# Optimization experiments

Measured on AMD Instinct MI355X. Metric: run time of the kernel, lower is better.

## Reference

```python
import jax, jax.numpy as jnp
import numpy as np

T, D, H, HD = 2048, 2048, 16, 128
ROPE_BASE = 10000.0
NEG = jnp.float32(-1e30)


def rms_norm(x):
    # F.rms_norm(x, (x.size(-1),)) with default eps = dtype eps
    eps = jnp.finfo(x.dtype).eps
    return x * jax.lax.rsqrt(jnp.mean(x * x, axis=-1, keepdims=True) + eps)


def rotary(x):
    # x: [1, T, H, hd]; half-split rotation as in Rotary.forward
    hd = x.shape[-1]
    inv_freq = (1.0 / ROPE_BASE) ** (jnp.arange(0, hd, 2, dtype=jnp.float32) / hd)
    t = jnp.arange(x.shape[1], dtype=jnp.float32)
    freqs = jnp.outer(t, inv_freq)                      # [T, hd/2]
    cos = jnp.cos(freqs)[None, :, None, :]
    sin = jnp.sin(freqs)[None, :, None, :]
    x1, x2 = jnp.split(x, 2, axis=-1)
    return jnp.concatenate([x1 * cos + x2 * sin, -x1 * sin + x2 * cos], axis=-1)


def setup_inputs() -> dict:
    key = jax.random.key(0)
    ks = jax.random.split(key, 10)
    w = lambda k, shape: jax.random.normal(k, shape, jnp.float32) * 0.02
    return {
        "x":  jax.random.normal(ks[0], (1, T, D), jnp.float32),
        "vi": jax.random.normal(ks[1], (1, T, H, HD), jnp.float32),
        "x0": jax.random.normal(ks[2], (1, T, D), jnp.float32),
        "wq": w(ks[3], (D, D)),
        "wk": w(ks[4], (D, D)),
        "wv": w(ks[5], (D, D)),
        "wo": w(ks[6], (D, D)),
        "lamb": jnp.float32(0.5),
        "lambdas": jnp.array([1.0, 0.0], jnp.float32),
        "w_fc": w(ks[7], (4 * D, D)),
        "w_proj": w(ks[8], (D, 4 * D)),
    }


def reference(x, vi, x0, wq, wk, wv, wo, lamb, lambdas, w_fc, w_proj):
    # Block: residual blend with initial embedding x0
    xb = lambdas[0] * x + lambdas[1] * x0
    xn = rms_norm(xb)

    # --- CausalSelfAttention ---
    q = (xn @ wq.T).reshape(1, T, H, HD)
    k = (xn @ wk.T).reshape(1, T, H, HD)
    v = (xn @ wv.T).reshape(1, T, H, HD)
    v = (1.0 - lamb) * v + lamb * vi                     # value-embedding blend
    q = rotary(rms_norm(q))
    k = rotary(rms_norm(k))

    scale = 1.0 / jnp.sqrt(jnp.float32(HD))              # flex_attention default scale
    scores = jnp.einsum('bqhd,bkhd->bhqk', q, k) * scale # [1,H,T,T]
    causal = jnp.tril(jnp.ones((T, T), bool))
    scores = jnp.where(causal[None, None], scores, NEG)
    attn = jax.nn.softmax(scores, axis=-1)
    y = jnp.einsum('bhqk,bkhd->bqhd', attn, v).reshape(1, T, D)
    a = y @ wo.T                                         # attention output REPLACES x (no residual)

    # --- MLP with squared ReLU ---
    h = rms_norm(a) @ w_fc.T
    h = jnp.square(jax.nn.relu(h))
    out = a + h @ w_proj.T
    return out
```

## Files before the change

### kernel.cpp

```cpp
#include <hip/hip_runtime.h>
#include <hip/hip_bf16.h>

typedef __bf16 bf16;
typedef __bf16 bf16x8 __attribute__((ext_vector_type(8)));
typedef float f32x4 __attribute__((ext_vector_type(4)));

#define DD 2048
#define DD2 4194304ull
#define G9_LDS 131072

__device__ __forceinline__ void glds16(const void* g, void* l) {
  __builtin_amdgcn_global_load_lds((const __attribute__((address_space(1))) void*)g,
                                   (__attribute__((address_space(3))) void*)l, 16, 0, 0);
}

__device__ __forceinline__ f32x4 mfma16(bf16x8 a, bf16x8 b, f32x4 c) {
  return __builtin_amdgcn_mfma_f32_16x16x32_bf16(a, b, c, 0, 0, 0);
}

__global__ __launch_bounds__(256) void cvt_all(const float* __restrict__ s0, const float* __restrict__ s1,
                                               const float* __restrict__ s2, const float* __restrict__ s3,
                                               const float* __restrict__ s4, const float* __restrict__ s5,
                                               bf16* __restrict__ dbase) {
  const int b = blockIdx.x;
  const float* src; bf16* dst; int lb;
  if (b < 8192)       { int r = b >> 11; src = (r == 0) ? s0 : (r == 1) ? s1 : (r == 2) ? s2 : s3;
                        dst = dbase + (size_t)r * DD2; lb = b & 2047; }
  else if (b < 16384) { src = s4; dst = dbase + 4 * DD2; lb = b - 8192; }
  else                { src = s5; dst = dbase + 8 * DD2; lb = b - 16384; }
  size_t i = ((size_t)lb * 256 + threadIdx.x) * 8;
  float4 a = *(const float4*)(src + i);
  float4 c = *(const float4*)(src + i + 4);
  bf16x8 o;
  o[0] = (bf16)a.x; o[1] = (bf16)a.y; o[2] = (bf16)a.z; o[3] = (bf16)a.w;
  o[4] = (bf16)c.x; o[5] = (bf16)c.y; o[6] = (bf16)c.z; o[7] = (bf16)c.w;
  *(bf16x8*)(dst + i) = o;
}

template<bool BLEND>
__global__ __launch_bounds__(256) void prenorm_k(const float* __restrict__ x, const float* __restrict__ x0,
                                                 const float* __restrict__ lambdas, bf16* __restrict__ out) {
  const int t = blockIdx.x, tid = threadIdx.x;
  const float4* xr = (const float4*)(x + (size_t)t * DD);
  float4 a0 = xr[2 * tid], a1 = xr[2 * tid + 1];
  float v[8] = {a0.x, a0.y, a0.z, a0.w, a1.x, a1.y, a1.z, a1.w};
  if (BLEND) {
    const float l0 = lambdas[0], l1 = lambdas[1];
    const float4* yr = (const float4*)(x0 + (size_t)t * DD);
    float4 b0 = yr[2 * tid], b1 = yr[2 * tid + 1];
    float w[8] = {b0.x, b0.y, b0.z, b0.w, b1.x, b1.y, b1.z, b1.w};
#pragma unroll
    for (int i = 0; i < 8; ++i) v[i] = l0 * v[i] + l1 * w[i];
  }
  float ss = 0.f;
#pragma unroll
  for (int i = 0; i < 8; ++i) ss += v[i] * v[i];
#pragma unroll
  for (int off = 1; off < 64; off <<= 1) ss += __shfl_xor(ss, off, 64);
  __shared__ float red[4];
  const int wid = tid >> 6;
  if ((tid & 63) == 0) red[wid] = ss;
  __syncthreads();
  ss = red[0] + red[1] + red[2] + red[3];
  const float sc = rsqrtf(ss * (1.0f / DD) + 1.1920928955078125e-07f);
  bf16x8 o;
#pragma unroll
  for (int i = 0; i < 8; ++i) o[i] = (bf16)(v[i] * sc);
  *(bf16x8*)(out + (size_t)t * DD + tid * 8) = o;
}

__global__ __launch_bounds__(256) void rope_k(bf16* __restrict__ qg, bf16* __restrict__ kg) {
  const int tid = threadIdx.x, lane = tid & 63, wid = tid >> 6;
  const int p = blockIdx.x * 4 + wid;
  bf16* base = ((p >> 15) ? kg : qg);
  const int t = (p >> 4) & 2047, hh = p & 15;
  base += (size_t)t * DD + hh * 128;
  float x1 = (float)base[lane], x2 = (float)base[lane + 64];
  float ss = x1 * x1 + x2 * x2;
#pragma unroll
  for (int off = 1; off < 64; off <<= 1) ss += __shfl_xor(ss, off, 64);
  const float sc = rsqrtf(ss * (1.0f / 128.0f) + 1.1920928955078125e-07f);
  x1 *= sc; x2 *= sc;
  const float fr = (float)t * exp2f((float)lane * (-13.287712379549449f / 64.0f));
  const float s = sinf(fr), c = cosf(fr);
  base[lane]      = (bf16)(x1 * c + x2 * s);
  base[lane + 64] = (bf16)(-x1 * s + x2 * c);
}

__global__ __launch_bounds__(256) void vt_k(const bf16* __restrict__ v, bf16* __restrict__ vt) {
  __shared__ alignas(16) bf16 tile[16 * 128];
  const int tb = blockIdx.x, hb = blockIdx.y, tid = threadIdx.x;
  glds16(v + (size_t)(tb * 16 + (tid >> 4)) * DD + hb * 128 + (tid & 15) * 8, tile + tid * 8);
  __syncthreads();
  const int d_l = tid & 127, tc = tid >> 7;
  bf16x8 o;
#pragma unroll
  for (int i = 0; i < 8; ++i) o[i] = tile[(tc * 8 + i) * 128 + d_l];
  *(bf16x8*)(vt + (size_t)(hb * 128 + d_l) * DD + tb * 16 + tc * 8) = o;
}

__device__ __forceinline__ void g9_stageA(const bf16* A, int Kstride, int row0, int k0,
                                          bf16* buf, int hm, int tid) {
#pragma unroll
  for (int i = 0; i < 2; ++i) {
    int e = tid + i * 512;
    int prl = e >> 3, slot = e & 7;
    int wm = prl >> 6, r63 = prl & 63;
    glds16(A + (size_t)(row0 + wm * 128 + hm * 64 + r63) * Kstride + k0 + ((slot ^ (prl & 7)) * 8),
           buf + hm * 8192 + e * 8);
  }
}
__device__ __forceinline__ void g9_stageB(const bf16* B, int Kstride, int col0, int k0,
                                          bf16* buf, int hn, int tid) {
#pragma unroll
  for (int i = 0; i < 2; ++i) {
    int e = tid + i * 512;
    int pbl = e >> 3, slot = e & 7;
    int wn = pbl >> 5, q = pbl & 31;
    glds16(B + (size_t)(col0 + wn * 64 + hn * 32 + q) * Kstride + k0 + ((slot ^ (pbl & 7)) * 8),
           buf + 16384 + hn * 8192 + e * 8);
  }
}

__device__ __forceinline__ void gemm9_core(const bf16* __restrict__ A, const bf16* __restrict__ B,
                                           int Kstride, int Klen, int row0, int col0,
                                           bf16* smem, f32x4 (&acc)[8][4]) {
  const int tid = threadIdx.x, lane = tid & 63, wid = tid >> 6;
  const int wm = wid >> 2, wn = wid & 3;
  const int l15 = lane & 15, g = lane >> 4;
  const int sw = l15 & 7;
  const int NT = Klen >> 6;
  g9_stageA(A, Kstride, row0, 0, smem, 0, tid);
  g9_stageB(B, Kstride, col0, 0, smem, 0, tid);
  g9_stageB(B, Kstride, col0, 0, smem, 1, tid);
  g9_stageA(A, Kstride, row0, 0, smem, 1, tid);

  bf16x8 a[4][2], b0[2][2], b1[2][2];
  for (int t = 0; t < NT; ++t) {
    bf16* cb = smem + (t & 1) * 32768;
    bf16* sb = smem + ((t + 1) & 1) * 32768;
    const int ks0 = (t + 1) << 6;
    const bool st = (t + 1) < NT;
    asm volatile("s_waitcnt vmcnt(4)" ::: "memory");
    __builtin_amdgcn_s_barrier();
#pragma unroll
    for (int mm = 0; mm < 4; ++mm)
#pragma unroll
      for (int ks = 0; ks < 2; ++ks) {
        int pr = wm * 64 + mm * 16 + l15;
        a[mm][ks] = *(const bf16x8*)(cb + pr * 64 + (((ks * 4 + g) ^ sw) * 8));
      }
#pragma unroll
    for (int nn = 0; nn < 2; ++nn)
#pragma unroll
      for (int ks = 0; ks < 2; ++ks) {
        int pb = wn * 32 + nn * 16 + l15;
        b0[nn][ks] = *(const bf16x8*)(cb + 16384 + pb * 64 + (((ks * 4 + g) ^ sw) * 8));
      }
    if (st) g9_stageA(A, Kstride, row0, ks0, sb, 0, tid);
    __builtin_amdgcn_s_setprio(1);
#pragma unroll
    for (int mm = 0; mm < 4; ++mm)
#pragma unroll
      for (int nn = 0; nn < 2; ++nn)
#pragma unroll
        for (int ks = 0; ks < 2; ++ks)
          acc[mm][nn] = mfma16(a[mm][ks], b0[nn][ks], acc[mm][nn]);
    __builtin_amdgcn_s_setprio(0);
    __builtin_amdgcn_s_barrier();
    if (st) { asm volatile("s_waitcnt vmcnt(4)" ::: "memory"); }
    else    { asm volatile("s_waitcnt vmcnt(2)" ::: "memory"); }
    __builtin_amdgcn_s_barrier();
#pragma unroll
    for (int nn = 0; nn < 2; ++nn)
#pragma unroll
      for (int ks = 0; ks < 2; ++ks) {
        int pb = 128 + wn * 32 + nn * 16 + l15;
        b1[nn][ks] = *(const bf16x8*)(cb + 16384 + pb * 64 + (((ks * 4 + g) ^ sw) * 8));
      }
    if (st) g9_stageB(B, Kstride, col0, ks0, sb, 0, tid);
    __builtin_amdgcn_s_setprio(1);
#pragma unroll
    for (int mm = 0; mm < 4; ++mm)
#pragma unroll
      for (int nn = 0; nn < 2; ++nn)
#pragma unroll
        for (int ks = 0; ks < 2; ++ks)
          acc[mm][2 + nn] = mfma16(a[mm][ks], b1[nn][ks], acc[mm][2 + nn]);
    __builtin_amdgcn_s_setprio(0);
    __builtin_amdgcn_s_barrier();
    if (st) { asm volatile("s_waitcnt vmcnt(4)" ::: "memory"); }
    else    { asm volatile("s_waitcnt vmcnt(0)" ::: "memory"); }
    __builtin_amdgcn_s_barrier();
#pragma unroll
    for (int mm = 0; mm < 4; ++mm)
#pragma unroll
      for (int ks = 0; ks < 2; ++ks) {
        int pr = 128 + wm * 64 + mm * 16 + l15;
        a[mm][ks] = *(const bf16x8*)(cb + pr * 64 + (((ks * 4 + g) ^ sw) * 8));
      }
    if (st) g9_stageB(B, Kstride, col0, ks0, sb, 1, tid);
    __builtin_amdgcn_s_setprio(1);
#pragma unroll
    for (int mm = 0; mm < 4; ++mm)
#pragma unroll
      for (int nn = 0; nn < 2; ++nn)
#pragma unroll
        for (int ks = 0; ks < 2; ++ks)
          acc[4 + mm][nn] = mfma16(a[mm][ks], b0[nn][ks], acc[4 + mm][nn]);
    __builtin_amdgcn_s_setprio(0);
    __builtin_amdgcn_s_barrier();
    if (st) g9_stageA(A, Kstride, row0, ks0, sb, 1, tid);
    __builtin_amdgcn_s_setprio(1);
#pragma unroll
    for (int mm = 0; mm < 4; ++mm)
#pragma unroll
      for (int nn = 0; nn < 2; ++nn)
#pragma unroll
        for (int ks = 0; ks < 2; ++ks)
          acc[4 + mm][2 + nn] = mfma16(a[mm][ks], b1[nn][ks], acc[4 + mm][2 + nn]);
    __builtin_amdgcn_s_setprio(0);
    __builtin_amdgcn_s_barrier();
  }
}

#define GEMM9_EPI(STMT)                                                        \
  { const int lane_ = threadIdx.x & 63, wid_ = threadIdx.x >> 6;               \
    const int l15_ = lane_ & 15, g_ = lane_ >> 4;                              \
    const int wm_ = wid_ >> 2, wn_ = wid_ & 3;                                 \
    _Pragma("unroll") for (int m = 0; m < 8; ++m)                              \
    _Pragma("unroll") for (int n = 0; n < 4; ++n)                              \
    _Pragma("unroll") for (int j = 0; j < 4; ++j) {                            \
      int grow = row0 + wm_ * 128 + (m >> 2) * 64 + (m & 3) * 16 + g_ * 4 + j; \
      int gcol = col0 + wn_ * 64 + (n >> 1) * 32 + (n & 1) * 16 + l15_;        \
      float vacc = acc[m][n][j];                                               \
      STMT; } }

__global__ __launch_bounds__(512, 1) void gemm9_qkv(const bf16* __restrict__ A,
    const bf16* __restrict__ Wq, const bf16* __restrict__ Wk, const bf16* __restrict__ Wv,
    bf16* __restrict__ oq, bf16* __restrict__ ok, bf16* __restrict__ ov,
    const float* __restrict__ vi, const float* __restrict__ lambp) {
  extern __shared__ bf16 smem9[];
  const int z = blockIdx.z;
  const bf16* B = (z == 0) ? Wq : (z == 1) ? Wk : Wv;
  bf16* out = (z == 0) ? oq : (z == 1) ? ok : ov;
  const int row0 = blockIdx.y * 256, col0 = blockIdx.x * 256;
  f32x4 acc[8][4] = {};
  gemm9_core(A, B, DD, DD, row0, col0, smem9, acc);
  if (z < 2) {
    GEMM9_EPI( out[(size_t)grow * DD + gcol] = (bf16)vacc; )
  } else {
    const float lam = *lambp;
    GEMM9_EPI( out[(size_t)grow * DD + gcol] =
                 (bf16)((1.0f - lam) * vacc + lam * vi[(size_t)grow * DD + gcol]); )
  }
}

template<int EPI>
__global__ __launch_bounds__(512, 1) void gemm9_ep(const bf16* __restrict__ A, const bf16* __restrict__ B,
                                                   void* __restrict__ outv, int N, int Kstride,
                                                   int KlenMain, int Ktot) {
  extern __shared__ bf16 smem9[];
  const int row0 = blockIdx.y * 256, col0 = blockIdx.x * 256;
  const int kofs = blockIdx.z * KlenMain;
  const int Klen = min(KlenMain, Ktot - kofs);
  f32x4 acc[8][4] = {};
  gemm9_core(A + kofs, B + kofs, Kstride, Klen, row0, col0, smem9, acc);
  if (EPI == 2) { float* out = (float*)outv + (size_t)blockIdx.z * DD2;
    GEMM9_EPI( out[(size_t)grow * N + gcol] = vacc; ) }
  if (EPI == 3) { bf16* out = (bf16*)outv;
    GEMM9_EPI( float r = fmaxf(vacc, 0.f); out[(size_t)grow * N + gcol] = (bf16)(r * r); ) }
}

__global__ __launch_bounds__(256) void wo_red_prenorm(const float* __restrict__ p, float* __restrict__ a_f,
                                                      bf16* __restrict__ an) {
  const int t = blockIdx.x, tid = threadIdx.x;
  const size_t base = (size_t)t * DD + tid * 8;
  float4 a0 = *(const float4*)(p + base),        a1 = *(const float4*)(p + base + 4);
  float4 b0 = *(const float4*)(p + DD2 + base),  b1 = *(const float4*)(p + DD2 + base + 4);
  float v[8] = {a0.x + b0.x, a0.y + b0.y, a0.z + b0.z, a0.w + b0.w,
                a1.x + b1.x, a1.y + b1.y, a1.z + b1.z, a1.w + b1.w};
  *(float4*)(a_f + base)     = make_float4(v[0], v[1], v[2], v[3]);
  *(float4*)(a_f + base + 4) = make_float4(v[4], v[5], v[6], v[7]);
  float ss = 0.f;
#pragma unroll
  for (int i = 0; i < 8; ++i) ss += v[i] * v[i];
#pragma unroll
  for (int off = 1; off < 64; off <<= 1) ss += __shfl_xor(ss, off, 64);
  __shared__ float red[4];
  if ((tid & 63) == 0) red[tid >> 6] = ss;
  __syncthreads();
  ss = red[0] + red[1] + red[2] + red[3];
  const float sc = rsqrtf(ss * (1.0f / DD) + 1.1920928955078125e-07f);
  bf16x8 o;
#pragma unroll
  for (int i = 0; i < 8; ++i) o[i] = (bf16)(v[i] * sc);
  *(bf16x8*)(an + base) = o;
}

__global__ __launch_bounds__(256) void proj_red(const float* __restrict__ p, const float* __restrict__ a_f,
                                                float* __restrict__ out) {
  const size_t base = ((size_t)blockIdx.x * 256 + threadIdx.x) * 8;
#pragma unroll
  for (int h = 0; h < 2; ++h) {
    size_t i = base + h * 4;
    float4 r = *(const float4*)(a_f + i);
    float4 u = *(const float4*)(p + i);
    float4 w = *(const float4*)(p + DD2 + i);
    float4 z = *(const float4*)(p + 2 * DD2 + i);
    *(float4*)(out + i) = make_float4(r.x + u.x + w.x + z.x, r.y + u.y + w.y + z.y,
                                      r.z + u.z + w.z + z.z, r.w + u.w + w.w + z.w);
  }
}

__global__ __launch_bounds__(256) void attn_k(const bf16* __restrict__ qg, const bf16* __restrict__ kg,
                                              const bf16* __restrict__ vtg, bf16* __restrict__ yg) {
  __shared__ alignas(16) bf16 Ks[32 * 128];
  __shared__ alignas(16) bf16 Vt[128 * 32];
  __shared__ alignas(16) bf16 Pl[4][16 * 32];
  const int h = blockIdx.y, qb = 31 - blockIdx.x;
  const int tid = threadIdx.x, lane = tid & 63, wid = tid >> 6;
  const int l15 = lane & 15, g = lane >> 4;
  const int qrow = qb * 64 + wid * 16;
  const float scale = 0.08838834764831845f;
  bf16x8 aQ[4];
  {
    const bf16* qp = qg + (size_t)(qrow + l15) * DD + h * 128 + g * 8;
#pragma unroll
    for (int kc = 0; kc < 4; ++kc) aQ[kc] = *(const bf16x8*)(qp + kc * 32);
  }
  f32x4 acc[8] = {};
  f32x4 l4 = {0.f, 0.f, 0.f, 0.f};
  const int nkt = qb * 2 + 2;
  for (int kt = 0; kt < nkt; ++kt) {
    const int kbase = kt * 32;
    __syncthreads();
#pragma unroll
    for (int r = 0; r < 2; ++r) {
      int e = tid + r * 256;
      int row = e >> 4, slot = e & 15;
      glds16(kg + (size_t)(kbase + row) * DD + h * 128 + ((slot ^ (row & 7)) * 8), Ks + e * 8);
    }
#pragma unroll
    for (int r = 0; r < 2; ++r) {
      int e = tid + r * 256;
      int d = e >> 2, slot = e & 3;
      glds16(vtg + (size_t)(h * 128 + d) * DD + kbase + ((slot ^ (d & 3)) * 8), Vt + e * 8);
    }
    __syncthreads();
    f32x4 S0 = {}, S1 = {};
#pragma unroll
    for (int kc = 0; kc < 4; ++kc) {
      int r0 = l15, r1 = 16 + l15;
      bf16x8 b0 = *(const bf16x8*)(Ks + r0 * 128 + (((kc * 4 + g) ^ (r0 & 7)) * 8));
      bf16x8 b1 = *(const bf16x8*)(Ks + r1 * 128 + (((kc * 4 + g) ^ (r1 & 7)) * 8));
      S0 = mfma16(aQ[kc], b0, S0);
      S1 = mfma16(aQ[kc], b1, S1);
    }
    const int k0i = kbase + l15, k1i = k0i + 16;
    f32x4 p0, p1;
#pragma unroll
    for (int j = 0; j < 4; ++j) {
      int q = qrow + g * 4 + j;
      p0[j] = (k0i <= q) ? __expf(S0[j] * scale) : 0.f;
      p1[j] = (k1i <= q) ? __expf(S1[j] * scale) : 0.f;
      l4[j] += p0[j] + p1[j];
    }
    const int c0 = (l15 >> 3) ^ g, c1 = (2 + (l15 >> 3)) ^ g, w7 = l15 & 7;
#pragma unroll
    for (int j = 0; j < 4; ++j) {
      Pl[wid][(g * 4 + j) * 32 + c0 * 8 + w7] = (bf16)p0[j];
      Pl[wid][(g * 4 + j) * 32 + c1 * 8 + w7] = (bf16)p1[j];
    }
    bf16x8 aP = *(const bf16x8*)(&Pl[wid][l15 * 32 + ((g ^ (l15 >> 2)) * 8)]);
#pragma unroll
    for (int dt = 0; dt < 8; ++dt) {
      int d = dt * 16 + l15;
      bf16x8 bV = *(const bf16x8*)(Vt + d * 32 + ((g ^ (d & 3)) * 8));
      acc[dt] = mfma16(aP, bV, acc[dt]);
    }
  }
#pragma unroll
  for (int off = 1; off < 16; off <<= 1)
#pragma unroll
    for (int j = 0; j < 4; ++j) l4[j] += __shfl_xor(l4[j], off, 64);
#pragma unroll
  for (int dt = 0; dt < 8; ++dt)
#pragma unroll
    for (int j = 0; j < 4; ++j) {
      int q = qrow + g * 4 + j;
      yg[(size_t)q * DD + h * 128 + dt * 16 + l15] = (bf16)(acc[dt][j] / l4[j]);
    }
}

extern "C" void kernel_launch(void* const* d_in, const int* in_sizes, int n_in,
                              void* d_out, int out_size, void* d_ws, size_t ws_size,
                              hipStream_t stream) {
  const float* x       = (const float*)d_in[0];
  const float* vi      = (const float*)d_in[1];
  const float* x0      = (const float*)d_in[2];
  const float* wq      = (const float*)d_in[3];
  const float* wk      = (const float*)d_in[4];
  const float* wv      = (const float*)d_in[5];
  const float* wo      = (const float*)d_in[6];
  const float* lamb    = (const float*)d_in[7];
  const float* lambdas = (const float*)d_in[8];
  const float* wfc     = (const float*)d_in[9];
  const float* wproj   = (const float*)d_in[10];
  float* out = (float*)d_out;

  (void)hipFuncSetAttribute(reinterpret_cast<const void*>(gemm9_qkv),
                            hipFuncAttributeMaxDynamicSharedMemorySize, G9_LDS);
  (void)hipFuncSetAttribute(reinterpret_cast<const void*>(gemm9_ep<2>),
                            hipFuncAttributeMaxDynamicSharedMemorySize, G9_LDS);
  (void)hipFuncSetAttribute(reinterpret_cast<const void*>(gemm9_ep<3>),
                            hipFuncAttributeMaxDynamicSharedMemorySize, G9_LDS);

  char* wsb = (char*)d_ws;
  size_t off = 0;
  auto alloc = [&](size_t bytes) { void* p = wsb + off; off = (off + bytes + 255) & ~(size_t)255; return p; };
  bf16* wq_b  = (bf16*)alloc(DD2 * 2);
  bf16* wk_b  = (bf16*)alloc(DD2 * 2);
  bf16* wv_b  = (bf16*)alloc(DD2 * 2);
  bf16* wo_b  = (bf16*)alloc(DD2 * 2);
  bf16* wfc_b = (bf16*)alloc(DD2 * 8);
  bf16* wpj_b = (bf16*)alloc(DD2 * 8);
  bf16* xn_b  = (bf16*)alloc(DD2 * 2);
  bf16* q_b   = (bf16*)alloc(DD2 * 2);
  bf16* k_b   = (bf16*)alloc(DD2 * 2);
  bf16* v_b   = (bf16*)alloc(DD2 * 2);
  bf16* y_b   = (bf16*)alloc(DD2 * 2);
  bf16* an_b  = (bf16*)alloc(DD2 * 2);
  float* part = (float*)xn_b;
  float* a_f  = (float*)alloc(DD2 * 4);
  bf16* h_b   = (bf16*)alloc(DD2 * 8);
  bf16* vt_b  = h_b;

  cvt_all<<<24576, 256, 0, stream>>>(wq, wk, wv, wo, wfc, wproj, (bf16*)wsb);
  prenorm_k<true><<<2048, 256, 0, stream>>>(x, x0, lambdas, xn_b);
  gemm9_qkv<<<dim3(8, 8, 3), 512, G9_LDS, stream>>>(xn_b, wq_b, wk_b, wv_b, q_b, k_b, v_b, vi, lamb);
  rope_k<<<16384, 256, 0, stream>>>(q_b, k_b);
  vt_k<<<dim3(128, 16), 256, 0, stream>>>(v_b, vt_b);
  attn_k<<<dim3(32, 16), 256, 0, stream>>>(q_b, k_b, vt_b, y_b);
  gemm9_ep<2><<<dim3(8, 8, 2), 512, G9_LDS, stream>>>(y_b, wo_b, (void*)part, DD, DD, 1024, DD);
  wo_red_prenorm<<<2048, 256, 0, stream>>>(part, a_f, an_b);
  gemm9_ep<3><<<dim3(32, 8, 1), 512, G9_LDS, stream>>>(an_b, wfc_b, (void*)h_b, 4 * DD, DD, DD, DD);
  gemm9_ep<2><<<dim3(8, 8, 3), 512, G9_LDS, stream>>>(h_b, wpj_b, (void*)part, DD, 4 * DD, 2752, 4 * DD);
  proj_red<<<2048, 256, 0, stream>>>(part, a_f, out);
}
```

Baseline: 407.2 us.

## Restructure GEMM barriers, triple-buffer attention K/V, shuffle P, rebalance split-K

The GEMM main loop is rescheduled so LDS fragment reads and the next-stage global loads are issued before each wait and barrier, which drops one barrier per phase. The attention kernel triple-buffers K and V tiles with async loads and computes S transposed, then moves P into MFMA operand layout with cross-lane shuffles instead of a round trip through LDS. The Wo and proj GEMMs now use four even split-K slices, writing partials into reused workspace (including the bf16 wfc weight buffer after it has been consumed), and the reduction kernels sum the extra partials. Together these aim to cut sync stalls and raise occupancy, at the cost of more partial-sum memory traffic and tighter waitcnt accounting.

```diff
diff --git a/kernel.cpp b/kernel.cpp
--- a/kernel.cpp
+++ b/kernel.cpp
@@ -4,6 +4,7 @@
 typedef __bf16 bf16;
 typedef __bf16 bf16x8 __attribute__((ext_vector_type(8)));
 typedef float f32x4 __attribute__((ext_vector_type(4)));
+typedef unsigned int u32x4 __attribute__((ext_vector_type(4)));
 
 #define DD 2048
 #define DD2 4194304ull
@@ -16,6 +17,12 @@
 
 __device__ __forceinline__ f32x4 mfma16(bf16x8 a, bf16x8 b, f32x4 c) {
   return __builtin_amdgcn_mfma_f32_16x16x32_bf16(a, b, c, 0, 0, 0);
+}
+
+__device__ __forceinline__ unsigned pk2(float lo, float hi) {
+  unsigned short a = __builtin_bit_cast(unsigned short, (bf16)lo);
+  unsigned short b = __builtin_bit_cast(unsigned short, (bf16)hi);
+  return (unsigned)a | ((unsigned)b << 16);
 }
 
 __global__ __launch_bounds__(256) void cvt_all(const float* __restrict__ s0, const float* __restrict__ s1,
@@ -134,6 +141,8 @@
   g9_stageB(B, Kstride, col0, 0, smem, 0, tid);
   g9_stageB(B, Kstride, col0, 0, smem, 1, tid);
   g9_stageA(A, Kstride, row0, 0, smem, 1, tid);
+  asm volatile("s_waitcnt vmcnt(4)" ::: "memory");
+  __builtin_amdgcn_s_barrier();
 
   bf16x8 a[4][2], b0[2][2], b1[2][2];
   for (int t = 0; t < NT; ++t) {
@@ -141,23 +150,20 @@
     bf16* sb = smem + ((t + 1) & 1) * 32768;
     const int ks0 = (t + 1) << 6;
     const bool st = (t + 1) < NT;
-    asm volatile("s_waitcnt vmcnt(4)" ::: "memory");
+#pragma unroll
+    for (int mm = 0; mm < 4; ++mm)
+#pragma unroll
+      for (int ks = 0; ks < 2; ++ks)
+        a[mm][ks] = *(const bf16x8*)(cb + (wm * 64 + mm * 16 + l15) * 64 + (((ks * 4 + g) ^ sw) * 8));
+#pragma unroll
+    for (int nn = 0; nn < 2; ++nn)
+#pragma unroll
+      for (int ks = 0; ks < 2; ++ks)
+        b0[nn][ks] = *(const bf16x8*)(cb + 16384 + (wn * 32 + nn * 16 + l15) * 64 + (((ks * 4 + g) ^ sw) * 8));
+    if (st) g9_stageA(A, Kstride, row0, ks0, sb, 0, tid);
+    if (st) { asm volatile("s_waitcnt vmcnt(4)" ::: "memory"); }
+    else    { asm volatile("s_waitcnt vmcnt(2)" ::: "memory"); }
     __builtin_amdgcn_s_barrier();
-#pragma unroll
-    for (int mm = 0; mm < 4; ++mm)
-#pragma unroll
-      for (int ks = 0; ks < 2; ++ks) {
-        int pr = wm * 64 + mm * 16 + l15;
-        a[mm][ks] = *(const bf16x8*)(cb + pr * 64 + (((ks * 4 + g) ^ sw) * 8));
-      }
-#pragma unroll
-    for (int nn = 0; nn < 2; ++nn)
-#pragma unroll
-      for (int ks = 0; ks < 2; ++ks) {
-        int pb = wn * 32 + nn * 16 + l15;
-        b0[nn][ks] = *(const bf16x8*)(cb + 16384 + pb * 64 + (((ks * 4 + g) ^ sw) * 8));
-      }
-    if (st) g9_stageA(A, Kstride, row0, ks0, sb, 0, tid);
     __builtin_amdgcn_s_setprio(1);
 #pragma unroll
     for (int mm = 0; mm < 4; ++mm)
@@ -167,18 +173,15 @@
         for (int ks = 0; ks < 2; ++ks)
           acc[mm][nn] = mfma16(a[mm][ks], b0[nn][ks], acc[mm][nn]);
     __builtin_amdgcn_s_setprio(0);
+#pragma unroll
+    for (int nn = 0; nn < 2; ++nn)
+#pragma unroll
+      for (int ks = 0; ks < 2; ++ks)
+        b1[nn][ks] = *(const bf16x8*)(cb + 16384 + 8192 + (wn * 32 + nn * 16 + l15) * 64 + (((ks * 4 + g) ^ sw) * 8));
+    if (st) g9_stageB(B, Kstride, col0, ks0, sb, 0, tid);
+    if (st) { asm volatile("s_waitcnt vmcnt(4)" ::: "memory"); }
+    else    { asm volatile("s_waitcnt vmcnt(0)" ::: "memory"); }
     __builtin_amdgcn_s_barrier();
-    if (st) { asm volatile("s_waitcnt vmcnt(4)" ::: "memory"); }
-    else    { asm volatile("s_waitcnt vmcnt(2)" ::: "memory"); }
-    __builtin_amdgcn_s_barrier();
-#pragma unroll
-    for (int nn = 0; nn < 2; ++nn)
-#pragma unroll
-      for (int ks = 0; ks < 2; ++ks) {
-        int pb = 128 + wn * 32 + nn * 16 + l15;
-        b1[nn][ks] = *(const bf16x8*)(cb + 16384 + pb * 64 + (((ks * 4 + g) ^ sw) * 8));
-      }
-    if (st) g9_stageB(B, Kstride, col0, ks0, sb, 0, tid);
     __builtin_amdgcn_s_setprio(1);
 #pragma unroll
     for (int mm = 0; mm < 4; ++mm)
@@ -188,18 +191,13 @@
         for (int ks = 0; ks < 2; ++ks)
           acc[mm][2 + nn] = mfma16(a[mm][ks], b1[nn][ks], acc[mm][2 + nn]);
     __builtin_amdgcn_s_setprio(0);
+#pragma unroll
+    for (int mm = 0; mm < 4; ++mm)
+#pragma unroll
+      for (int ks = 0; ks < 2; ++ks)
+        a[mm][ks] = *(const bf16x8*)(cb + 8192 + (wm * 64 + mm * 16 + l15) * 64 + (((ks * 4 + g) ^ sw) * 8));
+    if (st) g9_stageB(B, Kstride, col0, ks0, sb, 1, tid);
     __builtin_amdgcn_s_barrier();
-    if (st) { asm volatile("s_waitcnt vmcnt(4)" ::: "memory"); }
-    else    { asm volatile("s_waitcnt vmcnt(0)" ::: "memory"); }
-    __builtin_amdgcn_s_barrier();
-#pragma unroll
-    for (int mm = 0; mm < 4; ++mm)
-#pragma unroll
-      for (int ks = 0; ks < 2; ++ks) {
-        int pr = 128 + wm * 64 + mm * 16 + l15;
-        a[mm][ks] = *(const bf16x8*)(cb + pr * 64 + (((ks * 4 + g) ^ sw) * 8));
-      }
-    if (st) g9_stageB(B, Kstride, col0, ks0, sb, 1, tid);
     __builtin_amdgcn_s_setprio(1);
 #pragma unroll
     for (int mm = 0; mm < 4; ++mm)
@@ -209,8 +207,9 @@
         for (int ks = 0; ks < 2; ++ks)
           acc[4 + mm][nn] = mfma16(a[mm][ks], b0[nn][ks], acc[4 + mm][nn]);
     __builtin_amdgcn_s_setprio(0);
+    if (st) { g9_stageA(A, Kstride, row0, ks0, sb, 1, tid);
+              asm volatile("s_waitcnt vmcnt(4)" ::: "memory"); }
     __builtin_amdgcn_s_barrier();
-    if (st) g9_stageA(A, Kstride, row0, ks0, sb, 1, tid);
     __builtin_amdgcn_s_setprio(1);
 #pragma unroll
     for (int mm = 0; mm < 4; ++mm)
@@ -220,7 +219,6 @@
         for (int ks = 0; ks < 2; ++ks)
           acc[4 + mm][2 + nn] = mfma16(a[mm][ks], b1[nn][ks], acc[4 + mm][2 + nn]);
     __builtin_amdgcn_s_setprio(0);
-    __builtin_amdgcn_s_barrier();
   }
 }
 
@@ -256,30 +254,44 @@
   }
 }
 
-template<int EPI>
-__global__ __launch_bounds__(512, 1) void gemm9_ep(const bf16* __restrict__ A, const bf16* __restrict__ B,
-                                                   void* __restrict__ outv, int N, int Kstride,
-                                                   int KlenMain, int Ktot) {
+__global__ __launch_bounds__(512, 1) void gemm9_part(const bf16* __restrict__ A, const bf16* __restrict__ B,
+                                                     float* __restrict__ o1, float* __restrict__ o2,
+                                                     int zsw, int N, int Kstride, int Klen) {
   extern __shared__ bf16 smem9[];
   const int row0 = blockIdx.y * 256, col0 = blockIdx.x * 256;
-  const int kofs = blockIdx.z * KlenMain;
-  const int Klen = min(KlenMain, Ktot - kofs);
+  const int z = blockIdx.z, kofs = z * Klen;
+  float* out = (z < zsw) ? (o1 + (size_t)z * DD2) : (o2 + (size_t)(z - zsw) * DD2);
   f32x4 acc[8][4] = {};
   gemm9_core(A + kofs, B + kofs, Kstride, Klen, row0, col0, smem9, acc);
-  if (EPI == 2) { float* out = (float*)outv + (size_t)blockIdx.z * DD2;
-    GEMM9_EPI( out[(size_t)grow * N + gcol] = vacc; ) }
-  if (EPI == 3) { bf16* out = (bf16*)outv;
-    GEMM9_EPI( float r = fmaxf(vacc, 0.f); out[(size_t)grow * N + gcol] = (bf16)(r * r); ) }
-}
-
-__global__ __launch_bounds__(256) void wo_red_prenorm(const float* __restrict__ p, float* __restrict__ a_f,
-                                                      bf16* __restrict__ an) {
+  GEMM9_EPI( out[(size_t)grow * N + gcol] = vacc; )
+}
+
+__global__ __launch_bounds__(512, 1) void gemm9_relu(const bf16* __restrict__ A, const bf16* __restrict__ B,
+                                                     bf16* __restrict__ out, int N, int Kstride, int Klen) {
+  extern __shared__ bf16 smem9[];
+  const int row0 = blockIdx.y * 256, col0 = blockIdx.x * 256;
+  f32x4 acc[8][4] = {};
+  gemm9_core(A, B, Kstride, Klen, row0, col0, smem9, acc);
+  GEMM9_EPI( float r = fmaxf(vacc, 0.f); out[(size_t)grow * N + gcol] = (bf16)(r * r); )
+}
+
+__global__ __launch_bounds__(256) void wo_red_prenorm(const float* __restrict__ pa, const float* __restrict__ pb,
+                                                      float* __restrict__ a_f, bf16* __restrict__ an) {
   const int t = blockIdx.x, tid = threadIdx.x;
   const size_t base = (size_t)t * DD + tid * 8;
-  float4 a0 = *(const float4*)(p + base),        a1 = *(const float4*)(p + base + 4);
-  float4 b0 = *(const float4*)(p + DD2 + base),  b1 = *(const float4*)(p + DD2 + base + 4);
-  float v[8] = {a0.x + b0.x, a0.y + b0.y, a0.z + b0.z, a0.w + b0.w,
-                a1.x + b1.x, a1.y + b1.y, a1.z + b1.z, a1.w + b1.w};
+  float v[8];
+#pragma unroll
+  for (int h = 0; h < 2; ++h) {
+    size_t i = base + h * 4;
+    float4 r0 = *(const float4*)(pa + i);
+    float4 r1 = *(const float4*)(pa + DD2 + i);
+    float4 r2 = *(const float4*)(pb + i);
+    float4 r3 = *(const float4*)(pb + DD2 + i);
+    v[h*4+0] = r0.x + r1.x + r2.x + r3.x;
+    v[h*4+1] = r0.y + r1.y + r2.y + r3.y;
+    v[h*4+2] = r0.z + r1.z + r2.z + r3.z;
+    v[h*4+3] = r0.w + r1.w + r2.w + r3.w;
+  }
   *(float4*)(a_f + base)     = make_float4(v[0], v[1], v[2], v[3]);
   *(float4*)(a_f + base + 4) = make_float4(v[4], v[5], v[6], v[7]);
   float ss = 0.f;
@@ -298,29 +310,46 @@
   *(bf16x8*)(an + base) = o;
 }
 
-__global__ __launch_bounds__(256) void proj_red(const float* __restrict__ p, const float* __restrict__ a_f,
-                                                float* __restrict__ out) {
+__global__ __launch_bounds__(256) void proj_red(const float* __restrict__ pa, const float* __restrict__ pw,
+                                                const float* __restrict__ a_f, float* __restrict__ out) {
   const size_t base = ((size_t)blockIdx.x * 256 + threadIdx.x) * 8;
 #pragma unroll
   for (int h = 0; h < 2; ++h) {
     size_t i = base + h * 4;
     float4 r = *(const float4*)(a_f + i);
-    float4 u = *(const float4*)(p + i);
-    float4 w = *(const float4*)(p + DD2 + i);
-    float4 z = *(const float4*)(p + 2 * DD2 + i);
-    *(float4*)(out + i) = make_float4(r.x + u.x + w.x + z.x, r.y + u.y + w.y + z.y,
-                                      r.z + u.z + w.z + z.z, r.w + u.w + w.w + z.w);
+    float4 u = *(const float4*)(pa + i);
+    float4 w = *(const float4*)(pa + DD2 + i);
+    float4 z = *(const float4*)(pa + 2 * DD2 + i);
+    float4 y = *(const float4*)(pw + i);
+    *(float4*)(out + i) = make_float4(r.x + u.x + w.x + z.x + y.x,
+                                      r.y + u.y + w.y + z.y + y.y,
+                                      r.z + u.z + w.z + z.z + y.z,
+                                      r.w + u.w + w.w + z.w + y.w);
+  }
+}
+
+__device__ __forceinline__ void att_stageK(const bf16* kg, int h, int kt, bf16* dst, int tid) {
+#pragma unroll
+  for (int r = 0; r < 2; ++r) {
+    int e = tid + r * 256, row = e >> 4, slot = e & 15;
+    glds16(kg + (size_t)(kt * 32 + row) * DD + h * 128 + ((slot ^ (row & 7)) * 8), dst + e * 8);
+  }
+}
+__device__ __forceinline__ void att_stageV(const bf16* vtg, int h, int kt, bf16* dst, int tid) {
+#pragma unroll
+  for (int r = 0; r < 2; ++r) {
+    int e = tid + r * 256, d = e >> 2, slot = e & 3;
+    glds16(vtg + (size_t)(h * 128 + d) * DD + kt * 32 + ((slot ^ ((d >> 1) & 3)) * 8), dst + e * 8);
   }
 }
 
 __global__ __launch_bounds__(256) void attn_k(const bf16* __restrict__ qg, const bf16* __restrict__ kg,
                                               const bf16* __restrict__ vtg, bf16* __restrict__ yg) {
-  __shared__ alignas(16) bf16 Ks[32 * 128];
-  __shared__ alignas(16) bf16 Vt[128 * 32];
-  __shared__ alignas(16) bf16 Pl[4][16 * 32];
+  __shared__ alignas(16) bf16 Ks[3][32 * 128];
+  __shared__ alignas(16) bf16 Vt[3][128 * 32];
   const int h = blockIdx.y, qb = 31 - blockIdx.x;
   const int tid = threadIdx.x, lane = tid & 63, wid = tid >> 6;
-  const int l15 = lane & 15, g = lane >> 4;
+  const int l15 = lane & 15, g = lane >> 4, swl = l15 & 7;
   const int qrow = qb * 64 + wid * 16;
   const float scale = 0.08838834764831845f;
   bf16x8 aQ[4];
@@ -330,66 +359,75 @@
     for (int kc = 0; kc < 4; ++kc) aQ[kc] = *(const bf16x8*)(qp + kc * 32);
   }
   f32x4 acc[8] = {};
-  f32x4 l4 = {0.f, 0.f, 0.f, 0.f};
+  float lsum = 0.f;
   const int nkt = qb * 2 + 2;
+  att_stageK(kg, h, 0, Ks[0], tid);
+  att_stageV(vtg, h, 0, Vt[0], tid);
+  att_stageK(kg, h, 1, Ks[1], tid);
+  att_stageV(vtg, h, 1, Vt[1], tid);
+  asm volatile("s_waitcnt vmcnt(4)" ::: "memory");
+  __builtin_amdgcn_s_barrier();
+  int cur = 0;
   for (int kt = 0; kt < nkt; ++kt) {
     const int kbase = kt * 32;
-    __syncthreads();
-#pragma unroll
-    for (int r = 0; r < 2; ++r) {
-      int e = tid + r * 256;
-      int row = e >> 4, slot = e & 15;
-      glds16(kg + (size_t)(kbase + row) * DD + h * 128 + ((slot ^ (row & 7)) * 8), Ks + e * 8);
-    }
-#pragma unroll
-    for (int r = 0; r < 2; ++r) {
-      int e = tid + r * 256;
-      int d = e >> 2, slot = e & 3;
-      glds16(vtg + (size_t)(h * 128 + d) * DD + kbase + ((slot ^ (d & 3)) * 8), Vt + e * 8);
-    }
-    __syncthreads();
+    const int nb = (cur >= 1) ? cur - 1 : 2;
+    bf16x8 kf0[4], kf1[4];
+#pragma unroll
+    for (int kc = 0; kc < 4; ++kc) {
+      kf0[kc] = *(const bf16x8*)(Ks[cur] + l15 * 128 + (((kc * 4 + g) ^ swl) * 8));
+      kf1[kc] = *(const bf16x8*)(Ks[cur] + (16 + l15) * 128 + (((kc * 4 + g) ^ swl) * 8));
+    }
+    if (kt + 2 < nkt) { att_stageK(kg, h, kt + 2, Ks[nb], tid);
+                        att_stageV(vtg, h, kt + 2, Vt[nb], tid); }
     f32x4 S0 = {}, S1 = {};
 #pragma unroll
     for (int kc = 0; kc < 4; ++kc) {
-      int r0 = l15, r1 = 16 + l15;
-      bf16x8 b0 = *(const bf16x8*)(Ks + r0 * 128 + (((kc * 4 + g) ^ (r0 & 7)) * 8));
-      bf16x8 b1 = *(const bf16x8*)(Ks + r1 * 128 + (((kc * 4 + g) ^ (r1 & 7)) * 8));
-      S0 = mfma16(aQ[kc], b0, S0);
-      S1 = mfma16(aQ[kc], b1, S1);
-    }
-    const int k0i = kbase + l15, k1i = k0i + 16;
-    f32x4 p0, p1;
+      S0 = mfma16(kf0[kc], aQ[kc], S0);
+      S1 = mfma16(kf1[kc], aQ[kc], S1);
+    }
+    const int q = qrow + l15;
+    float p0[4], p1[4];
 #pragma unroll
     for (int j = 0; j < 4; ++j) {
-      int q = qrow + g * 4 + j;
-      p0[j] = (k0i <= q) ? __expf(S0[j] * scale) : 0.f;
-      p1[j] = (k1i <= q) ? __expf(S1[j] * scale) : 0.f;
-      l4[j] += p0[j] + p1[j];
-    }
-    const int c0 = (l15 >> 3) ^ g, c1 = (2 + (l15 >> 3)) ^ g, w7 = l15 & 7;
-#pragma unroll
-    for (int j = 0; j < 4; ++j) {
-      Pl[wid][(g * 4 + j) * 32 + c0 * 8 + w7] = (bf16)p0[j];
-      Pl[wid][(g * 4 + j) * 32 + c1 * 8 + w7] = (bf16)p1[j];
-    }
-    bf16x8 aP = *(const bf16x8*)(&Pl[wid][l15 * 32 + ((g ^ (l15 >> 2)) * 8)]);
+      int k0 = kbase + 4 * g + j;
+      p0[j] = (k0 <= q) ? __expf(S0[j] * scale) : 0.f;
+      p1[j] = (k0 + 16 <= q) ? __expf(S1[j] * scale) : 0.f;
+      lsum += p0[j] + p1[j];
+    }
+    unsigned w0 = pk2(p0[0], p0[1]), w1 = pk2(p0[2], p0[3]);
+    unsigned w2 = pk2(p1[0], p1[1]), w3 = pk2(p1[2], p1[3]);
+    const int s0l = (g & 1) * 32 + l15, s1l = s0l + 16;
+    const bool hi = g >= 2;
+    unsigned t00 = __shfl(w0, s0l, 64), t10 = __shfl(w1, s0l, 64);
+    unsigned t01 = __shfl(w0, s1l, 64), t11 = __shfl(w1, s1l, 64);
+    unsigned u00 = __shfl(w2, s0l, 64), u10 = __shfl(w3, s0l, 64);
+    unsigned u01 = __shfl(w2, s1l, 64), u11 = __shfl(w3, s1l, 64);
+    u32x4 av = { hi ? u00 : t00, hi ? u10 : t10, hi ? u01 : t01, hi ? u11 : t11 };
+    bf16x8 aP = __builtin_bit_cast(bf16x8, av);
 #pragma unroll
     for (int dt = 0; dt < 8; ++dt) {
       int d = dt * 16 + l15;
-      bf16x8 bV = *(const bf16x8*)(Vt + d * 32 + ((g ^ (d & 3)) * 8));
+      bf16x8 bV = *(const bf16x8*)(Vt[cur] + d * 32 + ((g ^ ((d >> 1) & 3)) * 8));
       acc[dt] = mfma16(aP, bV, acc[dt]);
     }
-  }
-#pragma unroll
-  for (int off = 1; off < 16; off <<= 1)
-#pragma unroll
-    for (int j = 0; j < 4; ++j) l4[j] += __shfl_xor(l4[j], off, 64);
+    if (kt + 1 < nkt) {
+      if (kt + 2 < nkt) { asm volatile("s_waitcnt vmcnt(4)" ::: "memory"); }
+      else              { asm volatile("s_waitcnt vmcnt(0)" ::: "memory"); }
+      __builtin_amdgcn_s_barrier();
+    }
+    cur = (cur == 2) ? 0 : cur + 1;
+  }
+  lsum += __shfl_xor(lsum, 16, 64);
+  lsum += __shfl_xor(lsum, 32, 64);
+  f32x4 linv;
+#pragma unroll
+  for (int j = 0; j < 4; ++j) linv[j] = 1.0f / __shfl(lsum, 4 * g + j, 64);
 #pragma unroll
   for (int dt = 0; dt < 8; ++dt)
 #pragma unroll
     for (int j = 0; j < 4; ++j) {
-      int q = qrow + g * 4 + j;
-      yg[(size_t)q * DD + h * 128 + dt * 16 + l15] = (bf16)(acc[dt][j] / l4[j]);
+      int q = qrow + 4 * g + j;
+      yg[(size_t)q * DD + h * 128 + dt * 16 + l15] = (bf16)(acc[dt][j] * linv[j]);
     }
 }
 
@@ -411,9 +449,9 @@
 
   (void)hipFuncSetAttribute(reinterpret_cast<const void*>(gemm9_qkv),
                             hipFuncAttributeMaxDynamicSharedMemorySize, G9_LDS);
-  (void)hipFuncSetAttribute(reinterpret_cast<const void*>(gemm9_ep<2>),
+  (void)hipFuncSetAttribute(reinterpret_cast<const void*>(gemm9_part),
                             hipFuncAttributeMaxDynamicSharedMemorySize, G9_LDS);
-  (void)hipFuncSetAttribute(reinterpret_cast<const void*>(gemm9_ep<3>),
+  (void)hipFuncSetAttribute(reinterpret_cast<const void*>(gemm9_relu),
                             hipFuncAttributeMaxDynamicSharedMemorySize, G9_LDS);
 
   char* wsb = (char*)d_ws;
@@ -431,10 +469,11 @@
   bf16* v_b   = (bf16*)alloc(DD2 * 2);
   bf16* y_b   = (bf16*)alloc(DD2 * 2);
   bf16* an_b  = (bf16*)alloc(DD2 * 2);
-  float* part = (float*)xn_b;
+  float* partA = (float*)xn_b;
   float* a_f  = (float*)alloc(DD2 * 4);
   bf16* h_b   = (bf16*)alloc(DD2 * 8);
   bf16* vt_b  = h_b;
+  float* partB = (float*)h_b;
 
   cvt_all<<<24576, 256, 0, stream>>>(wq, wk, wv, wo, wfc, wproj, (bf16*)wsb);
   prenorm_k<true><<<2048, 256, 0, stream>>>(x, x0, lambdas, xn_b);
@@ -442,9 +481,9 @@
   rope_k<<<16384, 256, 0, stream>>>(q_b, k_b);
   vt_k<<<dim3(128, 16), 256, 0, stream>>>(v_b, vt_b);
   attn_k<<<dim3(32, 16), 256, 0, stream>>>(q_b, k_b, vt_b, y_b);
-  gemm9_ep<2><<<dim3(8, 8, 2), 512, G9_LDS, stream>>>(y_b, wo_b, (void*)part, DD, DD, 1024, DD);
-  wo_red_prenorm<<<2048, 256, 0, stream>>>(part, a_f, an_b);
-  gemm9_ep<3><<<dim3(32, 8, 1), 512, G9_LDS, stream>>>(an_b, wfc_b, (void*)h_b, 4 * DD, DD, DD, DD);
-  gemm9_ep<2><<<dim3(8, 8, 3), 512, G9_LDS, stream>>>(h_b, wpj_b, (void*)part, DD, 4 * DD, 2752, 4 * DD);
-  proj_red<<<2048, 256, 0, stream>>>(part, a_f, out);
-}
+  gemm9_part<<<dim3(8, 8, 4), 512, G9_LDS, stream>>>(y_b, wo_b, partA, partB, 2, DD, DD, 512);
+  wo_red_prenorm<<<2048, 256, 0, stream>>>(partA, partB, a_f, an_b);
+  gemm9_relu<<<dim3(32, 8), 512, G9_LDS, stream>>>(an_b, wfc_b, h_b, 4 * DD, DD, DD);
+  gemm9_part<<<dim3(8, 8, 4), 512, G9_LDS, stream>>>(h_b, wpj_b, partA, (float*)wfc_b, 3, DD, 4 * DD, 2048);
+  proj_red<<<2048, 256, 0, stream>>>(partA, (float*)wfc_b, a_f, out);
+}
```

After: 386.8 us. 5.0% less time.
